# Optimization experiments

Hardware: AMD Instinct MI355X
Metric: run time of the kernel (lower is better)

## Reference

```python
import jax, jax.numpy as jnp
import numpy as np

LAYER_START = 4
WS = 2  # context_window_size
EPS = 1e-8


def _alpha_for_k(tf, idx):
    # tf: [L, D] per-token layer features; idx: static window row indices (last entry is k)
    Wm = tf[idx]                       # [w, D]
    w = Wm.shape[0]
    _, R = jnp.linalg.qr(Wm.T)         # reduced QR of [D, w] -> R: [w, w]
    r = R[:, -1]
    sub = R[:-1, :-1]
    coln = jnp.linalg.norm(sub, axis=0)
    align = jnp.mean(sub / coln, axis=1) @ R[:-1, -1] / jnp.linalg.norm(r[:-1])
    align = 1.0 / (align * w * 2)
    nov = jnp.abs(r[-1]) / jnp.linalg.norm(r)
    return align, nov


def _unify_token(tf):
    # tf: [L, D] -> pooled [D]
    L = tf.shape[0]
    aligns, novs = [], []
    for k in range(L):  # loop over small fixed layer count (structurally distinct windows)
        # NOTE: original torch code token_feature[k-ws:k] yields an EMPTY slice for k < ws
        left = list(range(k - WS, k)) if k >= WS else []
        right = list(range(k + 1, min(k + WS + 1, L)))
        idx = np.array(left + right + [k], dtype=np.int32)
        a, n = _alpha_for_k(tf, idx)
        aligns.append(a)
        novs.append(n)
    aa = jnp.stack(aligns)
    nv = jnp.stack(novs)
    aa = aa / aa.sum()
    nv = nv / nv.sum()
    alpha = aa + nv
    alpha = alpha / alpha.sum()
    return tf.T @ alpha


def _token_var(tf):
    # tf: [L, D] -> variance (unbiased) of subdiagonal of cosine-sim map
    w = jnp.linalg.norm(tf, axis=1, keepdims=True)
    sim = (tf @ tf.T) / jnp.clip(w * w.T, EPS)
    return jnp.var(jnp.diagonal(sim, -1), ddof=1)


def reference(all_hidden_states, attention_mask):
    # all_hidden_states: [B, num_layers, S, D]; attention_mask: [B, S] (all sentences equal length)
    T = int(np.asarray(attention_mask).sum(axis=1)[0]) - 1  # unmask_num = sum(mask) - 1
    sf = all_hidden_states[:, LAYER_START:, :T, :]          # [B, L, T, D]
    per_tok = jax.vmap(jax.vmap(_unify_token, in_axes=1))(sf)  # [B, T, D]

    def per_sentence(s, ose):
        v = jax.vmap(_token_var, in_axes=1)(s)  # [T]
        v = v / v.sum()
        return ose.T @ v                        # [D]

    return jax.vmap(per_sentence)(sf, per_tok)  # [B, D]


def setup_inputs():
    key = jax.random.key(0)
    all_hidden_states = jax.random.normal(key, (8, 12, 512, 768), dtype=jnp.float32)
    attention_mask = jnp.ones((8, 512), dtype=jnp.int32)
    return {"all_hidden_states": all_hidden_states, "attention_mask": attention_mask}
```

## Files before the change

kernel.cpp:

```cpp
#include <hip/hip_runtime.h>
#include <math.h>

#define NLAYER_TOT 12
#define LAYER0 4
#define SMAX 512
#define DIM 768

__global__ void k_init(const int* __restrict__ mask, int* __restrict__ wsT,
                       float* __restrict__ out) {
    __shared__ int red[512];
    int tid = threadIdx.x;
    red[tid] = mask[tid];
    __syncthreads();
    for (int s = 256; s >= 1; s >>= 1) {
        if (tid < s) red[tid] += red[tid + s];
        __syncthreads();
    }
    if (tid == 0) wsT[0] = red[0] - 1;
    for (int i = tid; i < 8 * DIM; i += 512) out[i] = 0.0f;
}

__global__ __launch_bounds__(64) void k_gram(const float* __restrict__ in,
                                             const int* __restrict__ wsT,
                                             float* __restrict__ Gout) {
    int T = wsT[0];
    int t = blockIdx.x;
    int b = blockIdx.y;
    if (t >= T) return;
    int lane = threadIdx.x;
    const float* base = in + ((size_t)(b * NLAYER_TOT + LAYER0) * SMAX + t) * DIM;
    float acc[36];
#pragma unroll
    for (int p = 0; p < 36; ++p) acc[p] = 0.0f;
#pragma unroll
    for (int it = 0; it < 3; ++it) {
        int d = it * 256 + lane * 4;
        float4 x[8];
#pragma unroll
        for (int k = 0; k < 8; ++k)
            x[k] = *(const float4*)(base + (size_t)k * SMAX * DIM + d);
        int p = 0;
#pragma unroll
        for (int i = 0; i < 8; ++i)
#pragma unroll
            for (int j = i; j < 8; ++j) {
                acc[p] += x[i].x * x[j].x + x[i].y * x[j].y + x[i].z * x[j].z + x[i].w * x[j].w;
                ++p;
            }
    }
    float* gdst = Gout + ((size_t)b * SMAX + t) * 36;
#pragma unroll
    for (int p = 0; p < 36; ++p) {
        float v = acc[p];
#pragma unroll
        for (int off = 32; off >= 1; off >>= 1) v += __shfl_xor(v, off, 64);
        if (lane == 0) gdst[p] = v;
    }
}

template <int W>
__device__ inline void alpha_nov(const float* __restrict__ Gf, const int* __restrict__ idx,
                                 float& align_o, float& nov_o) {
    float Gs[W][W];
#pragma unroll
    for (int i = 0; i < W; ++i)
#pragma unroll
        for (int j = i; j < W; ++j) {
            float v = Gf[idx[i] * 8 + idx[j]];
            Gs[i][j] = v;
            Gs[j][i] = v;
        }
    float R[W][W];
#pragma unroll
    for (int j = 0; j < W; ++j) {
#pragma unroll
        for (int i = 0; i <= j; ++i) {
            float s = Gs[i][j];
#pragma unroll
            for (int q = 0; q < i; ++q) s -= R[q][i] * R[q][j];
            R[i][j] = (i == j) ? sqrtf(s) : (s / R[i][i]);
        }
    }
    float ic[W - 1];
#pragma unroll
    for (int j = 0; j < W - 1; ++j) ic[j] = 1.0f / sqrtf(Gs[j][j]);
    float m[W - 1];
#pragma unroll
    for (int i = 0; i < W - 1; ++i) {
        float s = 0.0f;
#pragma unroll
        for (int j = i; j < W - 1; ++j) s += R[i][j] * ic[j];
        m[i] = s * (1.0f / (float)(W - 1));
    }
    float num = 0.0f, n1 = 0.0f;
#pragma unroll
    for (int i = 0; i < W - 1; ++i) {
        num += m[i] * R[i][W - 1];
        n1 += R[i][W - 1] * R[i][W - 1];
    }
    float align_raw = num / sqrtf(n1);
    align_o = 1.0f / (align_raw * (float)W * 2.0f);
    nov_o = fabsf(R[W - 1][W - 1]) / sqrtf(Gs[W - 1][W - 1]);
}

__global__ __launch_bounds__(64) void k_alpha(const int* __restrict__ wsT,
                                              const float* __restrict__ Gin,
                                              float* __restrict__ alpha,
                                              float* __restrict__ vraw) {
    int T = wsT[0];
    int id = blockIdx.x * 64 + threadIdx.x;
    int b = id >> 9;
    int t = id & 511;
    if (b >= 8 || t >= T) return;
    float Gf[64];
    const float* gsrc = Gin + ((size_t)b * SMAX + t) * 36;
    {
        int p = 0;
#pragma unroll
        for (int i = 0; i < 8; ++i)
#pragma unroll
            for (int j = i; j < 8; ++j) {
                float v = gsrc[p++];
                Gf[i * 8 + j] = v;
                Gf[j * 8 + i] = v;
            }
    }
    static constexpr int IDX0[5] = {1, 2, 0, 0, 0};
    static constexpr int IDX1[5] = {2, 3, 1, 0, 0};
    static constexpr int IDX2[5] = {0, 1, 3, 4, 2};
    static constexpr int IDX3[5] = {1, 2, 4, 5, 3};
    static constexpr int IDX4[5] = {2, 3, 5, 6, 4};
    static constexpr int IDX5[5] = {3, 4, 6, 7, 5};
    static constexpr int IDX6[5] = {4, 5, 7, 6, 0};
    static constexpr int IDX7[5] = {5, 6, 7, 0, 0};
    float a[8], n[8];
    alpha_nov<3>(Gf, IDX0, a[0], n[0]);
    alpha_nov<3>(Gf, IDX1, a[1], n[1]);
    alpha_nov<5>(Gf, IDX2, a[2], n[2]);
    alpha_nov<5>(Gf, IDX3, a[3], n[3]);
    alpha_nov<5>(Gf, IDX4, a[4], n[4]);
    alpha_nov<5>(Gf, IDX5, a[5], n[5]);
    alpha_nov<4>(Gf, IDX6, a[6], n[6]);
    alpha_nov<3>(Gf, IDX7, a[7], n[7]);
    float sa = 0.0f, sn = 0.0f;
#pragma unroll
    for (int k = 0; k < 8; ++k) { sa += a[k]; sn += n[k]; }
    float isa = 1.0f / sa, isn = 1.0f / sn;
    float al[8], ss = 0.0f;
#pragma unroll
    for (int k = 0; k < 8; ++k) { al[k] = a[k] * isa + n[k] * isn; ss += al[k]; }
    float iss = 1.0f / ss;
    float* adst = alpha + ((size_t)b * SMAX + t) * 8;
#pragma unroll
    for (int k = 0; k < 8; ++k) adst[k] = al[k] * iss;
    float c[7], mu = 0.0f;
#pragma unroll
    for (int i = 0; i < 7; ++i) {
        float denom = sqrtf(Gf[i * 8 + i]) * sqrtf(Gf[(i + 1) * 8 + (i + 1)]);
        denom = denom > 1e-8f ? denom : 1e-8f;
        c[i] = Gf[(i + 1) * 8 + i] / denom;
        mu += c[i];
    }
    mu *= (1.0f / 7.0f);
    float var = 0.0f;
#pragma unroll
    for (int i = 0; i < 7; ++i) var += (c[i] - mu) * (c[i] - mu);
    vraw[(size_t)b * SMAX + t] = var * (1.0f / 6.0f);
}

__global__ void k_weights(const int* __restrict__ wsT, const float* __restrict__ alpha,
                          const float* __restrict__ vraw, float* __restrict__ W) {
    int T = wsT[0];
    int b = blockIdx.x;
    int tid = threadIdx.x;
    __shared__ float red[256];
    float s = 0.0f;
    for (int t = tid; t < T; t += 256) s += vraw[(size_t)b * SMAX + t];
    red[tid] = s;
    __syncthreads();
    for (int k = 128; k >= 1; k >>= 1) {
        if (tid < k) red[tid] += red[tid + k];
        __syncthreads();
    }
    float inv = 1.0f / red[0];
    for (int t = tid; t < T; t += 256) {
        float v = vraw[(size_t)b * SMAX + t] * inv;
#pragma unroll
        for (int k = 0; k < 8; ++k)
            W[((size_t)b * SMAX + t) * 8 + k] = alpha[((size_t)b * SMAX + t) * 8 + k] * v;
    }
}

__global__ void k_out(const float* __restrict__ in, const int* __restrict__ wsT,
                      const float* __restrict__ W, float* __restrict__ out) {
    int T = wsT[0];
    int tseg = blockIdx.x;
    int dchunk = blockIdx.y;
    int b = blockIdx.z;
    int d = dchunk * 256 + threadIdx.x;
    int t0 = tseg * 16;
    int t1 = min(t0 + 16, T);
    if (t0 >= t1) return;
    const float* base = in + ((size_t)(b * NLAYER_TOT + LAYER0) * SMAX) * DIM + d;
    const float* wb = W + (size_t)b * SMAX * 8;
    float acc = 0.0f;
    for (int t = t0; t < t1; ++t) {
#pragma unroll
        for (int k = 0; k < 8; ++k)
            acc += wb[t * 8 + k] * base[((size_t)k * SMAX + t) * DIM];
    }
    atomicAdd(&out[b * DIM + d], acc);
}

extern "C" void kernel_launch(void* const* d_in, const int* in_sizes, int n_in,
                              void* d_out, int out_size, void* d_ws, size_t ws_size,
                              hipStream_t stream) {
    const float* hs = (const float*)d_in[0];
    const int* mask = (const int*)d_in[1];
    float* out = (float*)d_out;
    char* ws = (char*)d_ws;
    int* wsT = (int*)ws;
    float* G = (float*)(ws + 256);
    float* alpha = (float*)(ws + 256 + (size_t)8 * 512 * 36 * 4);
    float* vraw = (float*)(ws + 256 + (size_t)(8 * 512 * 36 + 8 * 512 * 8) * 4);
    float* W = (float*)(ws + 256 + (size_t)(8 * 512 * 36 + 8 * 512 * 8 + 8 * 512) * 4);

    k_init<<<1, 512, 0, stream>>>(mask, wsT, out);
    k_gram<<<dim3(SMAX - 1, 8), 64, 0, stream>>>(hs, wsT, G);
    k_alpha<<<64, 64, 0, stream>>>(wsT, G, alpha, vraw);
    k_weights<<<8, 256, 0, stream>>>(wsT, alpha, vraw, W);
    k_out<<<dim3(32, 3, 8), 256, 0, stream>>>(hs, wsT, W, out);
}
```

Measured before the change: 249.6 us.

## Prefetch gram loads, pack four tokens per block, use fast rcp/rsq intrinsics

```diff
diff --git a/kernel.cpp b/kernel.cpp
--- a/kernel.cpp
+++ b/kernel.cpp
@@ -5,6 +5,14 @@
 #define LAYER0 4
 #define SMAX 512
 #define DIM 768
+
+__host__ __device__ constexpr int gp(int i, int j) {
+    return (i <= j) ? (i * 8 - i * (i - 1) / 2 + (j - i))
+                    : (j * 8 - j * (j - 1) / 2 + (i - j));
+}
+
+__device__ inline float frcp(float x) { return __builtin_amdgcn_rcpf(x); }
+__device__ inline float frsq(float x) { return __builtin_amdgcn_rsqf(x); }
 
 __global__ void k_init(const int* __restrict__ mask, int* __restrict__ wsT,
                        float* __restrict__ out) {
@@ -20,33 +28,45 @@
     for (int i = tid; i < 8 * DIM; i += 512) out[i] = 0.0f;
 }
 
-__global__ __launch_bounds__(64) void k_gram(const float* __restrict__ in,
-                                             const int* __restrict__ wsT,
-                                             float* __restrict__ Gout) {
-    int T = wsT[0];
-    int t = blockIdx.x;
+__global__ __launch_bounds__(256) void k_gram(const float* __restrict__ in,
+                                              const int* __restrict__ wsT,
+                                              float* __restrict__ Gout) {
+    int T = wsT[0];
+    int wave = threadIdx.x >> 6;
+    int lane = threadIdx.x & 63;
+    int t = blockIdx.x * 4 + wave;
     int b = blockIdx.y;
     if (t >= T) return;
-    int lane = threadIdx.x;
     const float* base = in + ((size_t)(b * NLAYER_TOT + LAYER0) * SMAX + t) * DIM;
     float acc[36];
 #pragma unroll
     for (int p = 0; p < 36; ++p) acc[p] = 0.0f;
+
+    float4 cur[8], nxt[8];
+#pragma unroll
+    for (int k = 0; k < 8; ++k)
+        cur[k] = *(const float4*)(base + (size_t)k * SMAX * DIM + lane * 4);
 #pragma unroll
     for (int it = 0; it < 3; ++it) {
-        int d = it * 256 + lane * 4;
-        float4 x[8];
-#pragma unroll
-        for (int k = 0; k < 8; ++k)
-            x[k] = *(const float4*)(base + (size_t)k * SMAX * DIM + d);
+        if (it < 2) {
+            int d = (it + 1) * 256 + lane * 4;
+#pragma unroll
+            for (int k = 0; k < 8; ++k)
+                nxt[k] = *(const float4*)(base + (size_t)k * SMAX * DIM + d);
+        }
         int p = 0;
 #pragma unroll
         for (int i = 0; i < 8; ++i)
 #pragma unroll
             for (int j = i; j < 8; ++j) {
-                acc[p] += x[i].x * x[j].x + x[i].y * x[j].y + x[i].z * x[j].z + x[i].w * x[j].w;
+                acc[p] += cur[i].x * cur[j].x + cur[i].y * cur[j].y +
+                          cur[i].z * cur[j].z + cur[i].w * cur[j].w;
                 ++p;
             }
+        if (it < 2) {
+#pragma unroll
+            for (int k = 0; k < 8; ++k) cur[k] = nxt[k];
+        }
     }
     float* gdst = Gout + ((size_t)b * SMAX + t) * 36;
 #pragma unroll
@@ -59,14 +79,14 @@
 }
 
 template <int W>
-__device__ inline void alpha_nov(const float* __restrict__ Gf, const int* __restrict__ idx,
+__device__ inline void alpha_nov(const float (&A)[36], const int (&idx)[5],
                                  float& align_o, float& nov_o) {
     float Gs[W][W];
 #pragma unroll
     for (int i = 0; i < W; ++i)
 #pragma unroll
         for (int j = i; j < W; ++j) {
-            float v = Gf[idx[i] * 8 + idx[j]];
+            float v = A[gp(idx[i], idx[j])];
             Gs[i][j] = v;
             Gs[j][i] = v;
         }
@@ -78,12 +98,13 @@
             float s = Gs[i][j];
 #pragma unroll
             for (int q = 0; q < i; ++q) s -= R[q][i] * R[q][j];
-            R[i][j] = (i == j) ? sqrtf(s) : (s / R[i][i]);
+            if (i == j) R[i][j] = s * frsq(s);
+            else        R[i][j] = s * frcp(R[i][i]);
         }
     }
     float ic[W - 1];
 #pragma unroll
-    for (int j = 0; j < W - 1; ++j) ic[j] = 1.0f / sqrtf(Gs[j][j]);
+    for (int j = 0; j < W - 1; ++j) ic[j] = frsq(Gs[j][j]);
     float m[W - 1];
 #pragma unroll
     for (int i = 0; i < W - 1; ++i) {
@@ -98,9 +119,9 @@
         num += m[i] * R[i][W - 1];
         n1 += R[i][W - 1] * R[i][W - 1];
     }
-    float align_raw = num / sqrtf(n1);
-    align_o = 1.0f / (align_raw * (float)W * 2.0f);
-    nov_o = fabsf(R[W - 1][W - 1]) / sqrtf(Gs[W - 1][W - 1]);
+    float align_raw = num * frsq(n1);
+    align_o = frcp(align_raw * (float)W * 2.0f);
+    nov_o = fabsf(R[W - 1][W - 1]) * frsq(Gs[W - 1][W - 1]);
 }
 
 __global__ __launch_bounds__(64) void k_alpha(const int* __restrict__ wsT,
@@ -112,19 +133,10 @@
     int b = id >> 9;
     int t = id & 511;
     if (b >= 8 || t >= T) return;
-    float Gf[64];
+    float A[36];
     const float* gsrc = Gin + ((size_t)b * SMAX + t) * 36;
-    {
-        int p = 0;
-#pragma unroll
-        for (int i = 0; i < 8; ++i)
-#pragma unroll
-            for (int j = i; j < 8; ++j) {
-                float v = gsrc[p++];
-                Gf[i * 8 + j] = v;
-                Gf[j * 8 + i] = v;
-            }
-    }
+#pragma unroll
+    for (int p = 0; p < 36; ++p) A[p] = gsrc[p];
     static constexpr int IDX0[5] = {1, 2, 0, 0, 0};
     static constexpr int IDX1[5] = {2, 3, 1, 0, 0};
     static constexpr int IDX2[5] = {0, 1, 3, 4, 2};
@@ -134,31 +146,30 @@
     static constexpr int IDX6[5] = {4, 5, 7, 6, 0};
     static constexpr int IDX7[5] = {5, 6, 7, 0, 0};
     float a[8], n[8];
-    alpha_nov<3>(Gf, IDX0, a[0], n[0]);
-    alpha_nov<3>(Gf, IDX1, a[1], n[1]);
-    alpha_nov<5>(Gf, IDX2, a[2], n[2]);
-    alpha_nov<5>(Gf, IDX3, a[3], n[3]);
-    alpha_nov<5>(Gf, IDX4, a[4], n[4]);
-    alpha_nov<5>(Gf, IDX5, a[5], n[5]);
-    alpha_nov<4>(Gf, IDX6, a[6], n[6]);
-    alpha_nov<3>(Gf, IDX7, a[7], n[7]);
+    alpha_nov<3>(A, IDX0, a[0], n[0]);
+    alpha_nov<3>(A, IDX1, a[1], n[1]);
+    alpha_nov<5>(A, IDX2, a[2], n[2]);
+    alpha_nov<5>(A, IDX3, a[3], n[3]);
+    alpha_nov<5>(A, IDX4, a[4], n[4]);
+    alpha_nov<5>(A, IDX5, a[5], n[5]);
+    alpha_nov<4>(A, IDX6, a[6], n[6]);
+    alpha_nov<3>(A, IDX7, a[7], n[7]);
     float sa = 0.0f, sn = 0.0f;
 #pragma unroll
     for (int k = 0; k < 8; ++k) { sa += a[k]; sn += n[k]; }
-    float isa = 1.0f / sa, isn = 1.0f / sn;
+    float isa = frcp(sa), isn = frcp(sn);
     float al[8], ss = 0.0f;
 #pragma unroll
     for (int k = 0; k < 8; ++k) { al[k] = a[k] * isa + n[k] * isn; ss += al[k]; }
-    float iss = 1.0f / ss;
+    float iss = frcp(ss);
     float* adst = alpha + ((size_t)b * SMAX + t) * 8;
 #pragma unroll
     for (int k = 0; k < 8; ++k) adst[k] = al[k] * iss;
     float c[7], mu = 0.0f;
 #pragma unroll
     for (int i = 0; i < 7; ++i) {
-        float denom = sqrtf(Gf[i * 8 + i]) * sqrtf(Gf[(i + 1) * 8 + (i + 1)]);
-        denom = denom > 1e-8f ? denom : 1e-8f;
-        c[i] = Gf[(i + 1) * 8 + i] / denom;
+        float denom = A[gp(i, i)] * A[gp(i + 1, i + 1)];
+        c[i] = A[gp(i, i + 1)] * frsq(denom > 1e-16f ? denom : 1e-16f);
         mu += c[i];
     }
     mu *= (1.0f / 7.0f);
@@ -182,7 +193,7 @@
         if (tid < k) red[tid] += red[tid + k];
         __syncthreads();
     }
-    float inv = 1.0f / red[0];
+    float inv = frcp(red[0]);
     for (int t = tid; t < T; t += 256) {
         float v = vraw[(size_t)b * SMAX + t] * inv;
 #pragma unroll
@@ -203,13 +214,21 @@
     if (t0 >= t1) return;
     const float* base = in + ((size_t)(b * NLAYER_TOT + LAYER0) * SMAX) * DIM + d;
     const float* wb = W + (size_t)b * SMAX * 8;
-    float acc = 0.0f;
-    for (int t = t0; t < t1; ++t) {
+    float acc0 = 0.0f, acc1 = 0.0f;
+    int t = t0;
+    for (; t + 1 < t1; t += 2) {
+#pragma unroll
+        for (int k = 0; k < 8; ++k) {
+            acc0 += wb[t * 8 + k] * base[((size_t)k * SMAX + t) * DIM];
+            acc1 += wb[(t + 1) * 8 + k] * base[((size_t)k * SMAX + t + 1) * DIM];
+        }
+    }
+    if (t < t1) {
 #pragma unroll
         for (int k = 0; k < 8; ++k)
-            acc += wb[t * 8 + k] * base[((size_t)k * SMAX + t) * DIM];
-    }
-    atomicAdd(&out[b * DIM + d], acc);
+            acc0 += wb[t * 8 + k] * base[((size_t)k * SMAX + t) * DIM];
+    }
+    atomicAdd(&out[b * DIM + d], acc0 + acc1);
 }
 
 extern "C" void kernel_launch(void* const* d_in, const int* in_sizes, int n_in,
@@ -226,7 +245,7 @@
     float* W = (float*)(ws + 256 + (size_t)(8 * 512 * 36 + 8 * 512 * 8 + 8 * 512) * 4);
 
     k_init<<<1, 512, 0, stream>>>(mask, wsT, out);
-    k_gram<<<dim3(SMAX - 1, 8), 64, 0, stream>>>(hs, wsT, G);
+    k_gram<<<dim3(128, 8), 256, 0, stream>>>(hs, wsT, G);
     k_alpha<<<64, 64, 0, stream>>>(wsT, G, alpha, vraw);
     k_weights<<<8, 256, 0, stream>>>(wsT, alpha, vraw, W);
     k_out<<<dim3(32, 3, 8), 256, 0, stream>>>(hs, wsT, W, out);
```

Result: no change. 246.3 us (-1.3%).
